# Kernel optimization log

Measured on AMD Instinct MI355X. Metric: run time of the kernel, lower is better.

Reference implementation:

```python
import jax, jax.numpy as jnp
import numpy as np

NUM_NODES = 100_000
NUM_EDGES = 3_200_000
THETA = 1.0  # module hyperparameter (default 1.0)


def setup_inputs() -> dict:
    key = jax.random.key(0)
    k_v, k_src, k_dst, k_t1, k_t2, k_r = jax.random.split(key, 6)
    v = jax.random.normal(k_v, (NUM_NODES,), dtype=jnp.float32)
    src = jax.random.randint(k_src, (NUM_EDGES,), 0, NUM_NODES, dtype=jnp.int32)
    dst = jax.random.randint(k_dst, (NUM_EDGES,), 0, NUM_NODES, dtype=jnp.int32)
    theta_sd_1 = jax.random.normal(k_t1, (NUM_EDGES,), dtype=jnp.float32) * 0.1
    theta_sd_2 = jax.random.normal(k_t2, (NUM_EDGES,), dtype=jnp.float32) * 0.1
    # conductance = 1/resistance, resistance in (0.5, 2.0) -> conductance in (0.5, 2.0)
    conductance = 1.0 / jax.random.uniform(k_r, (NUM_EDGES,), dtype=jnp.float32, minval=0.5, maxval=2.0)
    return {"t": 0, "v": v, "src": src, "dst": dst,
            "theta_sd_1": theta_sd_1, "theta_sd_2": theta_sd_2,
            "conductance": conductance}


def reference(t, v, src, dst, theta_sd_1, theta_sd_2, conductance):
    # per-edge gated current: g(vs, vd) = relu(theta1*(vs - vd) + theta2)
    diff = v[src] - v[dst]                                   # [E]
    current = conductance * jax.nn.relu(theta_sd_1 * diff + theta_sd_2)  # [E]
    incoming = jax.ops.segment_sum(current, dst, num_segments=NUM_NODES)  # [N]
    outgoing = jax.ops.segment_sum(current, src, num_segments=NUM_NODES)  # [N]
    return (incoming - outgoing) / THETA
```

## Files before the change

kernel.cpp:

```cpp
#include <hip/hip_runtime.h>
#include <hip/hip_fp16.h>


#define TL      13
#define TILE    (1 << TL)
#define NTILES  13
#define NBINS   (NTILES * NTILES)
#define PA_BLK  1024
#define PA_EPT  4
#define PA_EPB  (PA_BLK * PA_EPT)
#define SCAP    56
#define PC_BLK  1024
#define NCOPY   (2 * NTILES)

typedef int      vi4 __attribute__((ext_vector_type(4)));
typedef float    vf4 __attribute__((ext_vector_type(4)));
typedef unsigned vu2 __attribute__((ext_vector_type(2)));

__device__ __forceinline__ unsigned f16b(float f) {
    return (unsigned)__half_as_ushort(__float2half(f));
}
__device__ __forceinline__ float f16v(unsigned u) {
    return __half2float(__ushort_as_half((unsigned short)(u & 0xFFFFu)));
}

__global__ __launch_bounds__(PA_BLK) void pa_kernel(
    const int*   __restrict__ src,
    const int*   __restrict__ dst,
    const float* __restrict__ t1,
    const float* __restrict__ t2,
    const float* __restrict__ cond,
    vu2*         __restrict__ recs,
    int E)
{
    __shared__ vu2 sbuf[NBINS][SCAP];
    __shared__ int scnt[NBINS];

    for (int i = threadIdx.x; i < NBINS; i += PA_BLK) scnt[i] = 0;
    __syncthreads();

    const int i0 = blockIdx.x * PA_EPB + (int)threadIdx.x * PA_EPT;

    #define PUT(S, D, T1, T2, C)                                              \
        {                                                                     \
            int bin = ((S) >> TL) * NTILES + ((D) >> TL);                     \
            vu2 rec;                                                          \
            rec.x = (((unsigned)(D) & (TILE - 1)) << TL) |                    \
                    ((unsigned)(S) & (TILE - 1));                             \
            rec.y = (f16b((C) * (T1)) << 16) | f16b((C) * (T2));              \
            int idx = atomicAdd(&scnt[bin], 1);                               \
            if (idx < SCAP) sbuf[bin][idx] = rec;                             \
        }

    if (i0 + PA_EPT <= E) {
        vi4 s4 = __builtin_nontemporal_load((const vi4*)(src  + i0));
        vi4 d4 = __builtin_nontemporal_load((const vi4*)(dst  + i0));
        vf4 a4 = __builtin_nontemporal_load((const vf4*)(t1   + i0));
        vf4 b4 = __builtin_nontemporal_load((const vf4*)(t2   + i0));
        vf4 c4 = __builtin_nontemporal_load((const vf4*)(cond + i0));
        PUT(s4.x, d4.x, a4.x, b4.x, c4.x)
        PUT(s4.y, d4.y, a4.y, b4.y, c4.y)
        PUT(s4.z, d4.z, a4.z, b4.z, c4.z)
        PUT(s4.w, d4.w, a4.w, b4.w, c4.w)
    } else {
        for (int i = i0; i < E && i < i0 + PA_EPT; ++i)
            PUT(src[i], dst[i], t1[i], t2[i], cond[i])
    }
    #undef PUT

    __syncthreads();
    vu2* g = recs + (size_t)blockIdx.x * NBINS * SCAP;
    for (int idx = threadIdx.x; idx < NBINS * SCAP; idx += PA_BLK) {
        const int r    = idx / SCAP;
        const int slot = idx - r * SCAP;
        vu2 val = (slot < min(scnt[r], SCAP)) ? sbuf[r][slot] : (vu2)(0u);
        __builtin_nontemporal_store(val, g + idx);
    }
}

__global__ __launch_bounds__(PC_BLK) void pc_kernel(
    const float* __restrict__ v,
    const vu2*   __restrict__ recs,
    float*       __restrict__ part,
    int N, int G)
{
    __shared__ __align__(16) float tS[TILE];
    __shared__ __align__(16) float tD[TILE];
    __shared__ __align__(16) float aS[TILE];
    __shared__ __align__(16) float aD[TILE];

    const int sb = blockIdx.x / NTILES;
    const int db = blockIdx.x % NTILES;
    const int baseS = sb << TL;
    const int baseD = db << TL;
    const int lenS = min(TILE, N - baseS);
    const int lenD = min(TILE, N - baseD);

    for (int i = threadIdx.x; i < TILE; i += PC_BLK) {
        tS[i] = (i < lenS) ? v[baseS + i] : 0.0f;
        tD[i] = (i < lenD) ? v[baseD + i] : 0.0f;
        aS[i] = 0.0f;
        aD[i] = 0.0f;
    }
    __syncthreads();

    const int binoff = sb * NTILES + db;
    const int total  = G * SCAP;

    for (int j = threadIdx.x; j < total; j += PC_BLK) {
        const int blk  = j / SCAP;
        const int slot = j - blk * SCAP;
        vu2 r = recs[((size_t)blk * NBINS + binoff) * SCAP + slot];
        const int   sl = (int)(r.x & (TILE - 1));
        const int   dl = (int)((r.x >> TL) & (TILE - 1));
        const float A  = f16v(r.y >> 16);
        const float B  = f16v(r.y);
        const float x  = fmaf(A, tS[sl] - tD[dl], B);
        if (x > 0.0f) {
            atomicAdd(&aS[sl], -x);
            atomicAdd(&aD[dl],  x);
        }
    }
    __syncthreads();

    if (lenS > 0) {
        float* p = part + (size_t)db * N + baseS;
        const int l4 = lenS & ~3;
        for (int i = (int)threadIdx.x * 4; i < l4; i += PC_BLK * 4)
            *(float4*)(p + i) = *(const float4*)&aS[i];
        for (int i = l4 + (int)threadIdx.x; i < lenS; i += PC_BLK)
            p[i] = aS[i];
    }
    if (lenD > 0) {
        float* p = part + (size_t)(NTILES + sb) * N + baseD;
        const int l4 = lenD & ~3;
        for (int i = (int)threadIdx.x * 4; i < l4; i += PC_BLK * 4)
            *(float4*)(p + i) = *(const float4*)&aD[i];
        for (int i = l4 + (int)threadIdx.x; i < lenD; i += PC_BLK)
            p[i] = aD[i];
    }
}

__global__ __launch_bounds__(256) void pe_kernel(
    const float* __restrict__ part, float* __restrict__ out, int N4)
{
    int n = blockIdx.x * blockDim.x + threadIdx.x;
    if (n < N4) {
        float4 sm = make_float4(0.f, 0.f, 0.f, 0.f);
        for (int c = 0; c < NCOPY; ++c) {
            float4 q = ((const float4*)part)[(size_t)c * N4 + n];
            sm.x += q.x; sm.y += q.y; sm.z += q.z; sm.w += q.w;
        }
        ((float4*)out)[n] = sm;
    }
}

__global__ __launch_bounds__(256) void pe_scalar_kernel(
    const float* __restrict__ part, float* __restrict__ out, int N)
{
    int n = blockIdx.x * blockDim.x + threadIdx.x;
    if (n < N) {
        float sm = 0.0f;
        for (int c = 0; c < NCOPY; ++c) sm += part[(size_t)c * N + n];
        out[n] = sm;
    }
}

__global__ __launch_bounds__(256) void atomic_fallback_kernel(
    const float* __restrict__ v, const int* __restrict__ src, const int* __restrict__ dst,
    const float* __restrict__ t1, const float* __restrict__ t2, const float* __restrict__ cond,
    float* __restrict__ out, int E)
{
    int i = blockIdx.x * blockDim.x + threadIdx.x;
    int stride = gridDim.x * blockDim.x;
    for (; i < E; i += stride) {
        int s = src[i], d = dst[i];
        float x = fmaf(t1[i], v[s] - v[d], t2[i]);
        if (x > 0.0f) {
            float c = cond[i] * x;
            atomicAdd(&out[d], c);
            atomicAdd(&out[s], -c);
        }
    }
}

extern "C" void kernel_launch(void* const* d_in, const int* in_sizes, int n_in,
                              void* d_out, int out_size, void* d_ws, size_t ws_size,
                              hipStream_t stream) {
    const float* v    = (const float*)d_in[1];
    const int*   src  = (const int*)  d_in[2];
    const int*   dst  = (const int*)  d_in[3];
    const float* t1   = (const float*)d_in[4];
    const float* t2   = (const float*)d_in[5];
    const float* cond = (const float*)d_in[6];
    float* out = (float*)d_out;
    const int E = in_sizes[2];
    const int N = out_size;

    const int G = (E + PA_EPB - 1) / PA_EPB;

    const size_t recBytes = (size_t)G * NBINS * SCAP * sizeof(vu2);
    const size_t parBytes = (size_t)NCOPY * N * sizeof(float);

    const bool ok = (N <= NTILES * TILE) && (E > 0) &&
                    (recBytes + parBytes <= ws_size);

    if (ok) {
        vu2*   recs = (vu2*)d_ws;
        float* part = (float*)((char*)d_ws + recBytes);

        pa_kernel<<<G, PA_BLK, 0, stream>>>(src, dst, t1, t2, cond, recs, E);

        pc_kernel<<<NBINS, PC_BLK, 0, stream>>>(v, recs, part, N, G);

        if ((N & 3) == 0) {
            const int N4 = N / 4;
            pe_kernel<<<(N4 + 255) / 256, 256, 0, stream>>>(part, out, N4);
        } else {
            pe_scalar_kernel<<<(N + 255) / 256, 256, 0, stream>>>(part, out, N);
        }
    } else {
        (void)hipMemsetAsync(out, 0, (size_t)N * sizeof(float), stream);
        int grid = (E + 255) / 256;
        if (grid > 2048) grid = 2048;
        atomic_fallback_kernel<<<grid, 256, 0, stream>>>(v, src, dst, t1, t2, cond, out, E);
    }
}
```

Baseline: 75.30 us.

## Compact binned records via global cursors and split each bin across blocks

```diff
diff --git a/kernel.cpp b/kernel.cpp
--- a/kernel.cpp
+++ b/kernel.cpp
@@ -2,16 +2,19 @@
 #include <hip/hip_fp16.h>
 
 
-#define TL      13
-#define TILE    (1 << TL)
-#define NTILES  13
-#define NBINS   (NTILES * NTILES)
-#define PA_BLK  1024
-#define PA_EPT  4
-#define PA_EPB  (PA_BLK * PA_EPT)
-#define SCAP    56
-#define PC_BLK  1024
-#define NCOPY   (2 * NTILES)
+#define TL        13
+#define TILE      (1 << TL)
+#define NTILES    13
+#define NBINS     (NTILES * NTILES)
+#define PA_BLK    1024
+#define PA_EPT    4
+#define PA_EPB    (PA_BLK * PA_EPT)
+#define SCAPL     56
+#define NREP      8
+#define CURSTRIDE 16
+#define PC_BLK    1024
+#define S_PC      3
+#define NCOPY     (2 * NTILES * S_PC)
 
 typedef int      vi4 __attribute__((ext_vector_type(4)));
 typedef float    vf4 __attribute__((ext_vector_type(4)));
@@ -31,10 +34,12 @@
     const float* __restrict__ t2,
     const float* __restrict__ cond,
     vu2*         __restrict__ recs,
-    int E)
-{
-    __shared__ vu2 sbuf[NBINS][SCAP];
+    int*         __restrict__ cursors,
+    int E, int SEGCAP)
+{
+    __shared__ vu2 sbuf[NBINS][SCAPL];
     __shared__ int scnt[NBINS];
+    __shared__ int gbase[NBINS];
 
     for (int i = threadIdx.x; i < NBINS; i += PA_BLK) scnt[i] = 0;
     __syncthreads();
@@ -49,7 +54,7 @@
                     ((unsigned)(S) & (TILE - 1));                             \
             rec.y = (f16b((C) * (T1)) << 16) | f16b((C) * (T2));              \
             int idx = atomicAdd(&scnt[bin], 1);                               \
-            if (idx < SCAP) sbuf[bin][idx] = rec;                             \
+            if (idx < SCAPL) sbuf[bin][idx] = rec;                            \
         }
 
     if (i0 + PA_EPT <= E) {
@@ -69,28 +74,42 @@
     #undef PUT
 
     __syncthreads();
-    vu2* g = recs + (size_t)blockIdx.x * NBINS * SCAP;
-    for (int idx = threadIdx.x; idx < NBINS * SCAP; idx += PA_BLK) {
-        const int r    = idx / SCAP;
-        const int slot = idx - r * SCAP;
-        vu2 val = (slot < min(scnt[r], SCAP)) ? sbuf[r][slot] : (vu2)(0u);
-        __builtin_nontemporal_store(val, g + idx);
+    const int rep = blockIdx.x & (NREP - 1);
+    if (threadIdx.x < NBINS) {
+        int c = min(scnt[threadIdx.x], SCAPL);
+        int b = atomicAdd(&cursors[(threadIdx.x * NREP + rep) * CURSTRIDE], c);
+        if (b > SEGCAP) b = SEGCAP;
+        if (b + c > SEGCAP) c = SEGCAP - b;
+        scnt[threadIdx.x]  = c;
+        gbase[threadIdx.x] = b;
+    }
+    __syncthreads();
+
+    const int wave = threadIdx.x >> 6;
+    const int lane = threadIdx.x & 63;
+    for (int r = wave; r < NBINS; r += (PA_BLK / 64)) {
+        const int c = scnt[r];
+        vu2* g = recs + (size_t)(r * NREP + rep) * SEGCAP + gbase[r];
+        for (int j = lane; j < c; j += 64) g[j] = sbuf[r][j];
     }
 }
 
 __global__ __launch_bounds__(PC_BLK) void pc_kernel(
     const float* __restrict__ v,
     const vu2*   __restrict__ recs,
+    const int*   __restrict__ cursors,
     float*       __restrict__ part,
-    int N, int G)
+    int N, int SEGCAP)
 {
     __shared__ __align__(16) float tS[TILE];
     __shared__ __align__(16) float tD[TILE];
     __shared__ __align__(16) float aS[TILE];
     __shared__ __align__(16) float aD[TILE];
 
-    const int sb = blockIdx.x / NTILES;
-    const int db = blockIdx.x % NTILES;
+    const int bin = blockIdx.x / S_PC;
+    const int s   = blockIdx.x % S_PC;
+    const int sb  = bin / NTILES;
+    const int db  = bin % NTILES;
     const int baseS = sb << TL;
     const int baseD = db << TL;
     const int lenS = min(TILE, N - baseS);
@@ -104,27 +123,28 @@
     }
     __syncthreads();
 
-    const int binoff = sb * NTILES + db;
-    const int total  = G * SCAP;
-
-    for (int j = threadIdx.x; j < total; j += PC_BLK) {
-        const int blk  = j / SCAP;
-        const int slot = j - blk * SCAP;
-        vu2 r = recs[((size_t)blk * NBINS + binoff) * SCAP + slot];
-        const int   sl = (int)(r.x & (TILE - 1));
-        const int   dl = (int)((r.x >> TL) & (TILE - 1));
-        const float A  = f16v(r.y >> 16);
-        const float B  = f16v(r.y);
-        const float x  = fmaf(A, tS[sl] - tD[dl], B);
-        if (x > 0.0f) {
-            atomicAdd(&aS[sl], -x);
-            atomicAdd(&aD[dl],  x);
+    for (int rep = 0; rep < NREP; ++rep) {
+        const int cnt = min(cursors[(bin * NREP + rep) * CURSTRIDE], SEGCAP);
+        const int j0  = (int)((long long)cnt * s       / S_PC);
+        const int j1  = (int)((long long)cnt * (s + 1) / S_PC);
+        const vu2* p  = recs + (size_t)(bin * NREP + rep) * SEGCAP;
+        for (int j = j0 + (int)threadIdx.x; j < j1; j += PC_BLK) {
+            vu2 r = p[j];
+            const int   sl = (int)(r.x & (TILE - 1));
+            const int   dl = (int)((r.x >> TL) & (TILE - 1));
+            const float A  = f16v(r.y >> 16);
+            const float B  = f16v(r.y);
+            const float x  = fmaf(A, tS[sl] - tD[dl], B);
+            if (x > 0.0f) {
+                atomicAdd(&aS[sl], -x);
+                atomicAdd(&aD[dl],  x);
+            }
         }
     }
     __syncthreads();
 
     if (lenS > 0) {
-        float* p = part + (size_t)db * N + baseS;
+        float* p = part + (size_t)(db * S_PC + s) * N + baseS;
         const int l4 = lenS & ~3;
         for (int i = (int)threadIdx.x * 4; i < l4; i += PC_BLK * 4)
             *(float4*)(p + i) = *(const float4*)&aS[i];
@@ -132,7 +152,7 @@
             p[i] = aS[i];
     }
     if (lenD > 0) {
-        float* p = part + (size_t)(NTILES + sb) * N + baseD;
+        float* p = part + (size_t)(NTILES * S_PC + sb * S_PC + s) * N + baseD;
         const int l4 = lenD & ~3;
         for (int i = (int)threadIdx.x * 4; i < l4; i += PC_BLK * 4)
             *(float4*)(p + i) = *(const float4*)&aD[i];
@@ -197,21 +217,29 @@
     const int E = in_sizes[2];
     const int N = out_size;
 
-    const int G = (E + PA_EPB - 1) / PA_EPB;
-
-    const size_t recBytes = (size_t)G * NBINS * SCAP * sizeof(vu2);
+    const int segMean = E / (NBINS * NREP);
+    const int SEGCAP  = ((segMean + segMean / 4 + 512) + 15) & ~15;
+
+    const size_t recBytes = (size_t)NBINS * NREP * SEGCAP * sizeof(vu2);
+    const size_t curBytes = (size_t)NBINS * NREP * CURSTRIDE * sizeof(int);
     const size_t parBytes = (size_t)NCOPY * N * sizeof(float);
 
     const bool ok = (N <= NTILES * TILE) && (E > 0) &&
-                    (recBytes + parBytes <= ws_size);
+                    (recBytes + curBytes + parBytes <= ws_size);
 
     if (ok) {
-        vu2*   recs = (vu2*)d_ws;
-        float* part = (float*)((char*)d_ws + recBytes);
-
-        pa_kernel<<<G, PA_BLK, 0, stream>>>(src, dst, t1, t2, cond, recs, E);
-
-        pc_kernel<<<NBINS, PC_BLK, 0, stream>>>(v, recs, part, N, G);
+        vu2*   recs    = (vu2*)d_ws;
+        int*   cursors = (int*)((char*)d_ws + recBytes);
+        float* part    = (float*)((char*)d_ws + recBytes + curBytes);
+
+        (void)hipMemsetAsync(cursors, 0, curBytes, stream);
+
+        const int G = (E + PA_EPB - 1) / PA_EPB;
+        pa_kernel<<<G, PA_BLK, 0, stream>>>(src, dst, t1, t2, cond,
+                                            recs, cursors, E, SEGCAP);
+
+        pc_kernel<<<NBINS * S_PC, PC_BLK, 0, stream>>>(v, recs, cursors, part,
+                                                       N, SEGCAP);
 
         if ((N & 3) == 0) {
             const int N4 = N / 4;
```

Result: faster. 73.36 us (-2.6%).
